# Kernel optimization log

Hardware: AMD Instinct MI355X
Metric: run time of the kernel (lower is better)

The kernel has to match this reference:

```python
import jax, jax.numpy as jnp
import numpy as np

NUM_HEADS = 16


def setup_inputs() -> dict:
    key = jax.random.key(0)
    ks = jax.random.split(key, 7)
    B, S, H = 2, 2048, 1024
    x = jax.random.normal(ks[0], (B, S, H), dtype=jnp.float32)
    y = jax.random.normal(ks[1], (B, S, H), dtype=jnp.float32)
    bias = jnp.zeros((B, 1, 1, S), dtype=jnp.float32)  # additive attention bias (padding mask)
    w_scale = 0.02
    wq = jax.random.normal(ks[2], (H, H), dtype=jnp.float32) * w_scale
    wk = jax.random.normal(ks[3], (H, H), dtype=jnp.float32) * w_scale
    wv = jax.random.normal(ks[4], (H, H), dtype=jnp.float32) * w_scale
    wo = jax.random.normal(ks[5], (H, H), dtype=jnp.float32) * w_scale
    return {"x": x, "y": y, "bias": bias, "wq": wq, "wk": wk, "wv": wv, "wo": wo}


def reference(x, y, bias, wq, wk, wv, wo):
    B, S, H = x.shape
    nh = NUM_HEADS
    dh = H // nh
    # QKV projections, split heads: [B, S, H] -> [B, nh, S, dh]
    q = jnp.einsum("bsh,hd->bsd", x, wq).reshape(B, S, nh, dh).transpose(0, 2, 1, 3)
    k = jnp.einsum("bsh,hd->bsd", y, wk).reshape(B, S, nh, dh).transpose(0, 2, 1, 3)
    v = jnp.einsum("bsh,hd->bsd", y, wv).reshape(B, S, nh, dh).transpose(0, 2, 1, 3)
    # Scale queries (tensor2tensor convention: q *= size_per_head ** -0.5)
    q = q * (dh ** -0.5)
    logits = jnp.einsum("bhqd,bhkd->bhqk", q, k) + bias  # [B, nh, S, S]
    weights = jax.nn.softmax(logits, axis=-1)
    # (attention_dropout = 0.0 -> identity)
    ctx = jnp.einsum("bhqk,bhkd->bhqd", weights, v)  # [B, nh, S, dh]
    ctx = ctx.transpose(0, 2, 1, 3).reshape(B, S, H)  # combine heads
    return jnp.einsum("bsh,hd->bsd", ctx, wo)
```

## Files before the change

kernel.cpp:

```cpp
#include <hip/hip_runtime.h>

using u16 = unsigned short;
using u32 = unsigned int;

typedef __bf16 bf16x8 __attribute__((ext_vector_type(8)));
typedef __bf16 bf16x4 __attribute__((ext_vector_type(4)));
typedef float f32x4 __attribute__((ext_vector_type(4)));
typedef u16 u16x4 __attribute__((ext_vector_type(4)));

#define GLD_LDS16(gp, lp)                                                                 \
  __builtin_amdgcn_global_load_lds((const __attribute__((address_space(1))) void*)(gp),   \
                                   (__attribute__((address_space(3))) void*)(lp), 16, 0, 0)

__device__ __forceinline__ u16 f2b(float f) {
  union { float f; u32 u; } v; v.f = f;
  return (u16)((v.u + 0x7fffu + ((v.u >> 16) & 1u)) >> 16);
}

__device__ __forceinline__ void pl32swap(u32& a, u32& b) {
  asm("v_permlane32_swap_b32 %0, %1" : "+v"(a), "+v"(b));
}
__device__ __forceinline__ void pl16swap(u32& a, u32& b) {
  asm("v_permlane16_swap_b32 %0, %1" : "+v"(a), "+v"(b));
}
__device__ __forceinline__ u32 cvtpk(float lo, float hi) {
  u32 d; asm("v_cvt_pk_bf16_f32 %0, %1, %2" : "=v"(d) : "v"(lo), "v"(hi));
  return d;
}

__global__ __launch_bounds__(256) void prep(
    const float* __restrict__ w0, const float* __restrict__ w1,
    const float* __restrict__ w2, const float* __restrict__ w3,
    u16* __restrict__ o0, u16* __restrict__ o1,
    u16* __restrict__ o2, u16* __restrict__ o3,
    const float* __restrict__ x, const float* __restrict__ y,
    u16* __restrict__ xb, u16* __restrict__ yb) {
  __shared__ float tile[64][65];
  int z = blockIdx.z;
  if (z < 4) {
    const float* src; u16* dst;
    switch (z) {
      case 0: src = w0; dst = o0; break;
      case 1: src = w1; dst = o1; break;
      case 2: src = w2; dst = o2; break;
      default: src = w3; dst = o3; break;
    }
    int bx = blockIdx.x * 64, by = blockIdx.y * 64;
    int tx = threadIdx.x & 63, ty = threadIdx.x >> 6;
    for (int r = ty; r < 64; r += 4)
      tile[r][tx] = src[(size_t)(by + r) * 1024 + bx + tx];
    __syncthreads();
    for (int r = ty; r < 64; r += 4)
      dst[(size_t)(bx + r) * 1024 + by + tx] = f2b(tile[tx][r]);
  } else {
    const float* src = (z == 4) ? x : y;
    u16* dst = (z == 4) ? xb : yb;
    size_t base = ((size_t)(blockIdx.y * 16 + blockIdx.x) * 256 + threadIdx.x) * 8;
    const size_t step = (size_t)256 * 256 * 8, total = (size_t)4096 * 1024;
    for (size_t i = base; i < total; i += step) {
      float4 f0 = *(const float4*)(src + i);
      float4 f1 = *(const float4*)(src + i + 4);
      bf16x8 v;
      v[0] = (__bf16)f0.x; v[1] = (__bf16)f0.y; v[2] = (__bf16)f0.z; v[3] = (__bf16)f0.w;
      v[4] = (__bf16)f1.x; v[5] = (__bf16)f1.y; v[6] = (__bf16)f1.z; v[7] = (__bf16)f1.w;
      *(bf16x8*)(dst + i) = v;
    }
  }
}

#define BM 128
#define BN 128
#define BK 64

__global__ __launch_bounds__(256) void gemm_qkv(
    const u16* __restrict__ xb, const u16* __restrict__ yb, const u16* __restrict__ wT,
    u16* __restrict__ Qb, u16* __restrict__ Kb, u16* __restrict__ Vb) {
  __shared__ __align__(16) u16 As[BM * BK];
  __shared__ __align__(16) u16 Bs[BN * BK];
  const int K = 1024;
  int region = blockIdx.y >> 3;
  const u16* A = (region == 0) ? xb : yb;
  const u16* BT = wT + (size_t)region * 1024 * 1024;
  float scale = (region == 0) ? 0.125f : 1.0f;
  int tid = threadIdx.x;
  int wave = tid >> 6, lane = tid & 63;
  int r = lane & 15, kg = lane >> 4;
  int bm = blockIdx.x * BM, bn = (blockIdx.y & 7) * BN;
  int wr = (wave >> 1) * 64, wc = (wave & 1) * 64;
  f32x4 acc[4][4] = {};

  const u16* Ag = A + (size_t)(bm + wave * 32 + (lane >> 3)) * K + (lane & 7) * 8;
  const u16* Bg = BT + (size_t)(bn + wave * 32 + (lane >> 3)) * K + (lane & 7) * 8;
  u16* Asb = As + wave * 32 * BK;
  u16* Bsb = Bs + wave * 32 * BK;

  for (int k0 = 0; k0 < K; k0 += BK) {
#pragma unroll
    for (int c = 0; c < 4; ++c) {
      GLD_LDS16(Ag + (size_t)c * 8 * K + k0, Asb + c * 8 * BK);
      GLD_LDS16(Bg + (size_t)c * 8 * K + k0, Bsb + c * 8 * BK);
    }
    __syncthreads();
#pragma unroll
    for (int kk = 0; kk < 2; ++kk) {
      bf16x8 af[4], bfv[4];
#pragma unroll
      for (int m = 0; m < 4; ++m)
        af[m] = *(const bf16x8*)&As[(wr + m * 16 + r) * BK + kk * 32 + kg * 8];
#pragma unroll
      for (int n = 0; n < 4; ++n)
        bfv[n] = *(const bf16x8*)&Bs[(wc + n * 16 + r) * BK + kk * 32 + kg * 8];
#pragma unroll
      for (int m = 0; m < 4; ++m)
#pragma unroll
        for (int n = 0; n < 4; ++n)
          acc[m][n] = __builtin_amdgcn_mfma_f32_16x16x32_bf16(af[m], bfv[n], acc[m][n], 0, 0, 0);
    }
    __syncthreads();
  }

  if (region == 2) {
#pragma unroll
    for (int m = 0; m < 4; ++m)
#pragma unroll
      for (int n = 0; n < 4; ++n) {
        int row0 = bm + wr + m * 16 + kg * 4;
        int col = bn + wc + n * 16 + r;
        int bb = row0 >> 11, s = row0 & 2047;
        int hh = col >> 6, dd = col & 63;
        u16x4 pk;
#pragma unroll
        for (int i = 0; i < 4; ++i) pk[i] = f2b(acc[m][n][i]);
        *(u16x4*)&Vb[((size_t)(bb * 16 + hh) * 64 + dd) * 2048 + s] = pk;
      }
  } else {
    u16* dst = (region == 0) ? Qb : Kb;
#pragma unroll
    for (int m = 0; m < 4; ++m)
#pragma unroll
      for (int n = 0; n < 4; ++n)
#pragma unroll
        for (int i = 0; i < 4; ++i) {
          int row = bm + wr + m * 16 + kg * 4 + i;
          int col = bn + wc + n * 16 + r;
          dst[(size_t)row * 1024 + col] = f2b(acc[m][n][i] * scale);
        }
  }
}

__global__ __launch_bounds__(256) void gemm_wo(
    const u16* __restrict__ A, const u16* __restrict__ BT, float* __restrict__ Cp,
    float scale) {
  __shared__ __align__(16) u16 As[BM * BK];
  __shared__ __align__(16) u16 Bs[64 * BK];
  const int K = 1024, N = 1024;
  int tid = threadIdx.x;
  int wave = tid >> 6, lane = tid & 63;
  int r = lane & 15, kg = lane >> 4;
  int lhi = lane >> 3, llo = lane & 7;
  int bm = blockIdx.x * BM, bn = blockIdx.y * 64;
  int wr = (wave >> 1) * 64, wc = (wave & 1) * 32;
  f32x4 acc[4][2] = {};

  const u16* Ag = A + (size_t)(bm + wave * 32 + lhi) * K + llo * 8;
  const u16* Bg = BT + (size_t)(bn + wave * 16 + lhi) * K + llo * 8;
  u16* Asb = As + wave * 32 * BK;
  u16* Bsb = Bs + wave * 16 * BK;

  for (int k0 = 0; k0 < K; k0 += BK) {
#pragma unroll
    for (int c = 0; c < 4; ++c)
      GLD_LDS16(Ag + (size_t)c * 8 * K + k0, Asb + c * 8 * BK);
#pragma unroll
    for (int c = 0; c < 2; ++c)
      GLD_LDS16(Bg + (size_t)c * 8 * K + k0, Bsb + c * 8 * BK);
    __syncthreads();
#pragma unroll
    for (int kk = 0; kk < 2; ++kk) {
      bf16x8 af[4], bfv[2];
#pragma unroll
      for (int m = 0; m < 4; ++m)
        af[m] = *(const bf16x8*)&As[(wr + m * 16 + r) * BK + kk * 32 + kg * 8];
#pragma unroll
      for (int n = 0; n < 2; ++n)
        bfv[n] = *(const bf16x8*)&Bs[(wc + n * 16 + r) * BK + kk * 32 + kg * 8];
#pragma unroll
      for (int m = 0; m < 4; ++m)
#pragma unroll
        for (int n = 0; n < 2; ++n)
          acc[m][n] = __builtin_amdgcn_mfma_f32_16x16x32_bf16(af[m], bfv[n], acc[m][n], 0, 0, 0);
    }
    __syncthreads();
  }

#pragma unroll
  for (int m = 0; m < 4; ++m)
#pragma unroll
    for (int n = 0; n < 2; ++n)
#pragma unroll
      for (int i = 0; i < 4; ++i) {
        int row = bm + wr + m * 16 + kg * 4 + i;
        int col = bn + wc + n * 16 + r;
        Cp[(size_t)row * N + col] = acc[m][n][i] * scale;
      }
}

__global__ __launch_bounds__(256) void flash_attn(
    const u16* __restrict__ Q, const u16* __restrict__ Km, const u16* __restrict__ VtG,
    const float* __restrict__ bias, u16* __restrict__ ctx) {
  const int S = 2048, H = 1024;
  __shared__ __align__(16) u16 Ks[2][64 * 64];
  __shared__ __align__(16) u16 Vs[2][64 * 64];
  int tid = threadIdx.x;
  int wave = tid >> 6, lane = tid & 63;
  int r = lane & 15, kg = lane >> 4;
  int h = blockIdx.x, b = blockIdx.y, qt = blockIdx.z;

  const u16* Qb = Q + (size_t)(b * S + qt * 64 + wave * 16 + r) * H + h * 64 + kg * 8;
  bf16x8 qa[2];
  qa[0] = *(const bf16x8*)(Qb);
  qa[1] = *(const bf16x8*)(Qb + 32);

  int lhi = lane >> 3, llo = lane & 7;
  int ksch = llo ^ lhi;
  const u16* KgB = Km + (size_t)b * S * H + h * 64;
  const u16* VgB = VtG + ((size_t)(b * 16 + h) * 64) * 2048;
  const float* biasB = bias + (size_t)b * S;

  float m_i = -1e30f, l_i = 0.f;
  f32x4 acc[4] = {};

  auto issueKV = [&](int kv0, int bi) {
#pragma unroll
    for (int c = 0; c < 2; ++c) {
      GLD_LDS16(KgB + (size_t)(kv0 + wave * 16 + c * 8 + lhi) * H + ksch * 8,
                &Ks[bi][wave * 16 * 64 + c * 8 * 64]);
      GLD_LDS16(VgB + (size_t)(wave * 16 + c * 8 + lhi) * 2048 + kv0 + ksch * 8,
                &Vs[bi][wave * 16 * 64 + c * 8 * 64]);
    }
  };
  auto issueB = [&](int kv0, f32x4* bv) {
#pragma unroll
    for (int n = 0; n < 4; ++n)
      bv[n] = *(const f32x4*)(biasB + kv0 + n * 16 + (kg << 2));
  };

  auto compute = [&](const u16* KsB, const u16* VsB, const f32x4* bv) {
    f32x4 sv[4] = {};
    __builtin_amdgcn_s_setprio(1);
#pragma unroll
    for (int kk = 0; kk < 2; ++kk)
#pragma unroll
      for (int n = 0; n < 4; ++n) {
        bf16x8 kb = *(const bf16x8*)&KsB[(n * 16 + r) * 64 +
                                         ((((kk << 2) + kg) ^ (r & 7)) << 3)];
        sv[n] = __builtin_amdgcn_mfma_f32_16x16x32_bf16(kb, qa[kk], sv[n], 0, 0, 0);
      }
    __builtin_amdgcn_s_setprio(0);

    f32x4 s4[4];
#pragma unroll
    for (int n = 0; n < 4; ++n) s4[n] = sv[n] + bv[n];
    float m0 = fmaxf(fmaxf(s4[0][0], s4[0][1]), fmaxf(s4[0][2], s4[0][3]));
    float m1 = fmaxf(fmaxf(s4[1][0], s4[1][1]), fmaxf(s4[1][2], s4[1][3]));
    float m2 = fmaxf(fmaxf(s4[2][0], s4[2][1]), fmaxf(s4[2][2], s4[2][3]));
    float m3 = fmaxf(fmaxf(s4[3][0], s4[3][1]), fmaxf(s4[3][2], s4[3][3]));
    float mx = fmaxf(fmaxf(m0, m1), fmaxf(m2, m3));
    mx = fmaxf(mx, __shfl_xor(mx, 16));
    mx = fmaxf(mx, __shfl_xor(mx, 32));
    float sc = 1.f;
    if (mx > m_i + 8.f) { sc = __expf(m_i - mx); l_i *= sc; m_i = mx; }
    if (__any(sc != 1.f)) {
#pragma unroll
      for (int i = 0; i < 4; ++i) {
        float sci = __shfl(sc, (lane & 48) | ((kg << 2) + i));
#pragma unroll
        for (int n = 0; n < 4; ++n) acc[n][i] *= sci;
      }
    }
    float rs = 0.f;
    float e[4][4];
#pragma unroll
    for (int n = 0; n < 4; ++n)
#pragma unroll
      for (int i = 0; i < 4; ++i) {
        e[n][i] = __expf(s4[n][i] - m_i);
        rs += e[n][i];
      }
    rs += __shfl_xor(rs, 16);
    rs += __shfl_xor(rs, 32);
    l_i += rs;

    u32 w[4][2];
#pragma unroll
    for (int n = 0; n < 4; ++n) {
      w[n][0] = cvtpk(e[n][0], e[n][1]);
      w[n][1] = cvtpk(e[n][2], e[n][3]);
    }

    __builtin_amdgcn_s_setprio(1);
#pragma unroll
    for (int kk = 0; kk < 2; ++kk) {
      u32 a0 = w[2 * kk][0], a1 = w[2 * kk][1];
      u32 b0 = w[2 * kk + 1][0], b1 = w[2 * kk + 1][1];
      pl32swap(a0, b0); pl32swap(a1, b1);
      pl16swap(a0, b0); pl16swap(a1, b1);
      union { u32 u[4]; bf16x8 v; } pa;
      pa.u[0] = a0; pa.u[1] = a1; pa.u[2] = b0; pa.u[3] = b1;
#pragma unroll
      for (int n = 0; n < 4; ++n) {
        bf16x8 vb = *(const bf16x8*)&VsB[(n * 16 + r) * 64 +
                                         ((((kk << 2) + kg) ^ (r & 7)) << 3)];
        acc[n] = __builtin_amdgcn_mfma_f32_16x16x32_bf16(pa.v, vb, acc[n], 0, 0, 0);
      }
    }
    __builtin_amdgcn_s_setprio(0);
  };

  f32x4 bp[4], bn2[4];

  issueKV(0, 0); issueB(0, bp);
  __syncthreads();

  for (int t2 = 0; t2 < 16; ++t2) {
    int kv1 = (t2 * 2 + 1) * 64;
    int kv2 = ((t2 * 2 + 2) & 31) * 64;
    issueKV(kv1, 1); issueB(kv1, bn2);
    compute(Ks[0], Vs[0], bp);
    __syncthreads();
    issueKV(kv2, 0); issueB(kv2, bp);
    compute(Ks[1], Vs[1], bn2);
    __syncthreads();
  }

#pragma unroll
  for (int i = 0; i < 4; ++i) {
    float li = __shfl(l_i, (lane & 48) | ((kg << 2) + i));
    float inv = 1.0f / li;
    size_t row = (size_t)(b * S + qt * 64 + wave * 16 + (kg << 2) + i);
#pragma unroll
    for (int n = 0; n < 4; ++n)
      ctx[row * H + h * 64 + n * 16 + r] = f2b(acc[n][i] * inv);
  }
}

extern "C" void kernel_launch(void* const* d_in, const int* in_sizes, int n_in,
                              void* d_out, int out_size, void* d_ws, size_t ws_size,
                              hipStream_t stream) {
  const float* x    = (const float*)d_in[0];
  const float* y    = (const float*)d_in[1];
  const float* bias = (const float*)d_in[2];
  const float* wq   = (const float*)d_in[3];
  const float* wk   = (const float*)d_in[4];
  const float* wv   = (const float*)d_in[5];
  const float* wo   = (const float*)d_in[6];
  float* out = (float*)d_out;

  u16* ws = (u16*)d_ws;
  const size_t WELEM = 1024 * 1024;
  const size_t MELEM = (size_t)4096 * 1024;
  u16* wqT = ws;
  u16* wkT = wqT + WELEM;
  u16* wvT = wkT + WELEM;
  u16* woT = wvT + WELEM;
  u16* Qb  = woT + WELEM;
  u16* Kb  = Qb + MELEM;
  u16* Vb  = Kb + MELEM;
  u16* xb  = Vb + MELEM;
  u16* yb  = xb + MELEM;
  u16* Cb  = Qb;

  dim3 blk(256);
  prep<<<dim3(16, 16, 6), blk, 0, stream>>>(wq, wk, wv, wo, wqT, wkT, wvT, woT,
                                            x, y, xb, yb);
  gemm_qkv<<<dim3(32, 24), blk, 0, stream>>>(xb, yb, wqT, Qb, Kb, Vb);
  flash_attn<<<dim3(16, 2, 32), blk, 0, stream>>>(Qb, Kb, Vb, bias, Cb);
  gemm_wo<<<dim3(32, 16), blk, 0, stream>>>(Cb, woT, out, 1.0f);
}
```

Measured before the change: 158.9 us.

## Use 128-row query tiles with 8 waves and exp2-based softmax

Flash attention blocks now run 8 waves over 128 query rows, so each K/V tile loaded into LDS is shared by twice as many queries and each wave issues half as many global-to-LDS loads. The log2(e) factor is folded into the Q projection scale and into a prescaled copy of the bias made in the prep kernel, which lets the softmax use the native exp2 instruction instead of __expf. The cost is an extra prep slice, extra workspace for the scaled bias, and half as many attention blocks, which may reduce occupancy or load balance across CUs.

```diff
diff --git a/kernel.cpp b/kernel.cpp
--- a/kernel.cpp
+++ b/kernel.cpp
@@ -27,6 +27,7 @@
   u32 d; asm("v_cvt_pk_bf16_f32 %0, %1, %2" : "=v"(d) : "v"(lo), "v"(hi));
   return d;
 }
+#define EXP2(x) __builtin_amdgcn_exp2f(x)
 
 __global__ __launch_bounds__(256) void prep(
     const float* __restrict__ w0, const float* __restrict__ w1,
@@ -34,7 +35,8 @@
     u16* __restrict__ o0, u16* __restrict__ o1,
     u16* __restrict__ o2, u16* __restrict__ o3,
     const float* __restrict__ x, const float* __restrict__ y,
-    u16* __restrict__ xb, u16* __restrict__ yb) {
+    u16* __restrict__ xb, u16* __restrict__ yb,
+    const float* __restrict__ bias, float* __restrict__ bs) {
   __shared__ float tile[64][65];
   int z = blockIdx.z;
   if (z < 4) {
@@ -52,7 +54,7 @@
     __syncthreads();
     for (int r = ty; r < 64; r += 4)
       dst[(size_t)(bx + r) * 1024 + by + tx] = f2b(tile[tx][r]);
-  } else {
+  } else if (z < 6) {
     const float* src = (z == 4) ? x : y;
     u16* dst = (z == 4) ? xb : yb;
     size_t base = ((size_t)(blockIdx.y * 16 + blockIdx.x) * 256 + threadIdx.x) * 8;
@@ -65,6 +67,10 @@
       v[4] = (__bf16)f1.x; v[5] = (__bf16)f1.y; v[6] = (__bf16)f1.z; v[7] = (__bf16)f1.w;
       *(bf16x8*)(dst + i) = v;
     }
+  } else {
+    if (blockIdx.x == 0 && blockIdx.y == 0)
+      for (int i = threadIdx.x; i < 4096; i += 256)
+        bs[i] = bias[i] * 1.44269504088896f;
   }
 }
 
@@ -81,7 +87,7 @@
   int region = blockIdx.y >> 3;
   const u16* A = (region == 0) ? xb : yb;
   const u16* BT = wT + (size_t)region * 1024 * 1024;
-  float scale = (region == 0) ? 0.125f : 1.0f;
+  float scale = (region == 0) ? 0.125f * 1.44269504088896f : 1.0f;
   int tid = threadIdx.x;
   int wave = tid >> 6, lane = tid & 63;
   int r = lane & 15, kg = lane >> 4;
@@ -205,9 +211,9 @@
       }
 }
 
-__global__ __launch_bounds__(256) void flash_attn(
+__global__ __launch_bounds__(512) void flash_attn(
     const u16* __restrict__ Q, const u16* __restrict__ Km, const u16* __restrict__ VtG,
-    const float* __restrict__ bias, u16* __restrict__ ctx) {
+    const float* __restrict__ biasS, u16* __restrict__ ctx) {
   const int S = 2048, H = 1024;
   __shared__ __align__(16) u16 Ks[2][64 * 64];
   __shared__ __align__(16) u16 Vs[2][64 * 64];
@@ -216,7 +222,7 @@
   int r = lane & 15, kg = lane >> 4;
   int h = blockIdx.x, b = blockIdx.y, qt = blockIdx.z;
 
-  const u16* Qb = Q + (size_t)(b * S + qt * 64 + wave * 16 + r) * H + h * 64 + kg * 8;
+  const u16* Qb = Q + (size_t)(b * S + qt * 128 + wave * 16 + r) * H + h * 64 + kg * 8;
   bf16x8 qa[2];
   qa[0] = *(const bf16x8*)(Qb);
   qa[1] = *(const bf16x8*)(Qb + 32);
@@ -225,19 +231,16 @@
   int ksch = llo ^ lhi;
   const u16* KgB = Km + (size_t)b * S * H + h * 64;
   const u16* VgB = VtG + ((size_t)(b * 16 + h) * 64) * 2048;
-  const float* biasB = bias + (size_t)b * S;
+  const float* biasB = biasS + (size_t)b * S;
 
   float m_i = -1e30f, l_i = 0.f;
   f32x4 acc[4] = {};
 
   auto issueKV = [&](int kv0, int bi) {
-#pragma unroll
-    for (int c = 0; c < 2; ++c) {
-      GLD_LDS16(KgB + (size_t)(kv0 + wave * 16 + c * 8 + lhi) * H + ksch * 8,
-                &Ks[bi][wave * 16 * 64 + c * 8 * 64]);
-      GLD_LDS16(VgB + (size_t)(wave * 16 + c * 8 + lhi) * 2048 + kv0 + ksch * 8,
-                &Vs[bi][wave * 16 * 64 + c * 8 * 64]);
-    }
+    GLD_LDS16(KgB + (size_t)(kv0 + wave * 8 + lhi) * H + ksch * 8,
+              &Ks[bi][wave * 8 * 64]);
+    GLD_LDS16(VgB + (size_t)(wave * 8 + lhi) * 2048 + kv0 + ksch * 8,
+              &Vs[bi][wave * 8 * 64]);
   };
   auto issueB = [&](int kv0, f32x4* bv) {
 #pragma unroll
@@ -269,7 +272,7 @@
     mx = fmaxf(mx, __shfl_xor(mx, 16));
     mx = fmaxf(mx, __shfl_xor(mx, 32));
     float sc = 1.f;
-    if (mx > m_i + 8.f) { sc = __expf(m_i - mx); l_i *= sc; m_i = mx; }
+    if (mx > m_i + 8.f) { sc = EXP2(m_i - mx); l_i *= sc; m_i = mx; }
     if (__any(sc != 1.f)) {
 #pragma unroll
       for (int i = 0; i < 4; ++i) {
@@ -284,7 +287,7 @@
     for (int n = 0; n < 4; ++n)
 #pragma unroll
       for (int i = 0; i < 4; ++i) {
-        e[n][i] = __expf(s4[n][i] - m_i);
+        e[n][i] = EXP2(s4[n][i] - m_i);
         rs += e[n][i];
       }
     rs += __shfl_xor(rs, 16);
@@ -337,7 +340,7 @@
   for (int i = 0; i < 4; ++i) {
     float li = __shfl(l_i, (lane & 48) | ((kg << 2) + i));
     float inv = 1.0f / li;
-    size_t row = (size_t)(b * S + qt * 64 + wave * 16 + (kg << 2) + i);
+    size_t row = (size_t)(b * S + qt * 128 + wave * 16 + (kg << 2) + i);
 #pragma unroll
     for (int n = 0; n < 4; ++n)
       ctx[row * H + h * 64 + n * 16 + r] = f2b(acc[n][i] * inv);
@@ -368,12 +371,13 @@
   u16* Vb  = Kb + MELEM;
   u16* xb  = Vb + MELEM;
   u16* yb  = xb + MELEM;
+  float* bs = (float*)(yb + MELEM);
   u16* Cb  = Qb;
 
   dim3 blk(256);
-  prep<<<dim3(16, 16, 6), blk, 0, stream>>>(wq, wk, wv, wo, wqT, wkT, wvT, woT,
-                                            x, y, xb, yb);
+  prep<<<dim3(16, 16, 7), blk, 0, stream>>>(wq, wk, wv, wo, wqT, wkT, wvT, woT,
+                                            x, y, xb, yb, bias, bs);
   gemm_qkv<<<dim3(32, 24), blk, 0, stream>>>(xb, yb, wqT, Qb, Kb, Vb);
-  flash_attn<<<dim3(16, 2, 32), blk, 0, stream>>>(Qb, Kb, Vb, bias, Cb);
+  flash_attn<<<dim3(16, 2, 16), dim3(512), 0, stream>>>(Qb, Kb, Vb, bs, Cb);
   gemm_wo<<<dim3(32, 16), blk, 0, stream>>>(Cb, woT, out, 1.0f);
 }
```

New measurement: 140.7 us. 1.13x faster.
